# Kernel optimization log

Measured on AMD Instinct MI355X. Metric: run time of the kernel, lower is better.

Reference implementation:

```python
import jax, jax.numpy as jnp
import numpy as np

C = 16      # internal_channel
G = 8       # deform groups
KK = 9      # 3x3 kernel taps


def conv2d(x, w, b, pad):
    y = jax.lax.conv_general_dilated(
        x, w, window_strides=(1, 1), padding=[(pad, pad), (pad, pad)],
        dimension_numbers=('NCHW', 'OIHW', 'NCHW'))
    return y + b[None, :, None, None]


def feature_extraction(img, p):
    f1 = jax.nn.relu(conv2d(img, p['conv1_w'], p['conv1_b'], 1))   # [B,C,H,W]
    f2 = jax.nn.relu(conv2d(f1, p['conv2_w'], p['conv2_b'], 0))    # [B,C,H-2,W-2]
    f3 = jax.nn.relu(conv2d(f2, p['conv3_w'], p['conv3_b'], 0))    # [B,C,H-4,W-4]
    return [f1, f2, f3]


def deform_conv2d(x, offset, w, b, groups):
    # torchvision deform_conv2d semantics: stride 1, pad 1, dilation 1, 3x3,
    # zero out-of-bounds bilinear sampling, explicit offsets.
    B, Ci, H, W = x.shape
    Cg = Ci // groups
    off = offset.reshape(B, groups, KK, 2, H, W)
    oy, ox = off[:, :, :, 0], off[:, :, :, 1]          # [B,G,K,H,W]
    k = jnp.arange(KK)
    ky = (k // 3).reshape(1, 1, KK, 1, 1).astype(x.dtype)
    kx = (k % 3).reshape(1, 1, KK, 1, 1).astype(x.dtype)
    hh = jnp.arange(H, dtype=x.dtype).reshape(1, 1, 1, H, 1)
    ww = jnp.arange(W, dtype=x.dtype).reshape(1, 1, 1, 1, W)
    ys = hh - 1.0 + ky + oy                            # sample rows
    xs = ww - 1.0 + kx + ox                            # sample cols
    y0 = jnp.floor(ys); x0 = jnp.floor(xs)
    dy = ys - y0; dx = xs - x0
    y0i = y0.astype(jnp.int32); x0i = x0.astype(jnp.int32)
    xg = x.reshape(B, groups, Cg, H * W)

    def gather(iy, ix):
        valid = ((iy >= 0) & (iy < H) & (ix >= 0) & (ix < W)).astype(x.dtype)
        idx = jnp.clip(iy, 0, H - 1) * W + jnp.clip(ix, 0, W - 1)
        g = jnp.take_along_axis(xg, idx.reshape(B, groups, 1, KK * H * W), axis=3)
        return g.reshape(B, groups, Cg, KK, H, W) * valid[:, :, None]

    v = (gather(y0i, x0i) * ((1 - dy) * (1 - dx))[:, :, None]
         + gather(y0i, x0i + 1) * ((1 - dy) * dx)[:, :, None]
         + gather(y0i + 1, x0i) * (dy * (1 - dx))[:, :, None]
         + gather(y0i + 1, x0i + 1) * (dy * dx)[:, :, None])
    v = v.reshape(B, Ci, KK, H, W)
    out = jnp.einsum('ocK,bcKhw->bohw', w.reshape(w.shape[0], Ci, KK), v)
    return out + b[None, :, None, None]


def setup_inputs() -> dict:
    key = jax.random.key(0)
    ks = jax.random.split(key, 12)
    B, H, Wd = 4, 256, 256
    d = {
        'ref_image': jax.random.normal(ks[0], (B, 3, H, Wd), jnp.float32),
        'unreg_image': jax.random.normal(ks[1], (B, 3, H, Wd), jnp.float32),
        'conv1_w': jax.random.normal(ks[2], (C, 3, 3, 3), jnp.float32) * 0.05,
        'conv1_b': jnp.zeros((C,), jnp.float32),
        'conv2_w': jax.random.normal(ks[3], (C, C, 3, 3), jnp.float32) * 0.05,
        'conv2_b': jnp.zeros((C,), jnp.float32),
        'conv3_w': jax.random.normal(ks[4], (C, C, 3, 3), jnp.float32) * 0.05,
        'conv3_b': jnp.zeros((C,), jnp.float32),
        'off1_w': jax.random.normal(ks[5], (2 * G * KK, 2 * C, 3, 3), jnp.float32) * 0.01,
        'off1_b': jnp.zeros((2 * G * KK,), jnp.float32),
        'off2_w': jax.random.normal(ks[6], (2 * G * KK, 2 * C, 3, 3), jnp.float32) * 0.01,
        'off2_b': jnp.zeros((2 * G * KK,), jnp.float32),
        'off3_w': jax.random.normal(ks[7], (2 * G * KK, 2 * C, 3, 3), jnp.float32) * 0.01,
        'off3_b': jnp.zeros((2 * G * KK,), jnp.float32),
        'dcn_w': jax.random.normal(ks[8], (C, C, 3, 3), jnp.float32) * 0.05,
        'dcn_b': jnp.zeros((C,), jnp.float32),
    }
    return d


def reference(ref_image, unreg_image, conv1_w, conv1_b, conv2_w, conv2_b,
              conv3_w, conv3_b, off1_w, off1_b, off2_w, off2_b,
              off3_w, off3_b, dcn_w, dcn_b):
    p = dict(conv1_w=conv1_w, conv1_b=conv1_b, conv2_w=conv2_w, conv2_b=conv2_b,
             conv3_w=conv3_w, conv3_b=conv3_b)
    ref_f = feature_extraction(ref_image, p)
    unr_f = feature_extraction(unreg_image, p)
    off_ws = [(off1_w, off1_b), (off2_w, off2_b), (off3_w, off3_b)]
    aligned = []
    for i in range(3):
        cat = jnp.concatenate([ref_f[i], unr_f[i]], axis=1)          # [B,2C,Hi,Wi]
        offset = jax.nn.relu(conv2d(cat, off_ws[i][0], off_ws[i][1], 1))
        aligned.append(deform_conv2d(unr_f[i], offset, dcn_w, dcn_b, G))
    return tuple(aligned)
```

## Files before the change

### kernel.cpp

```cpp
#include <hip/hip_runtime.h>


typedef __attribute__((ext_vector_type(8))) short bf16x8;
typedef __attribute__((ext_vector_type(4))) float f32x4;
typedef __attribute__((ext_vector_type(2))) float f32x2;

__device__ inline unsigned short f2bf(float f) {
    union { float f; unsigned int u; } x; x.f = f;
    unsigned int u = x.u;
    u += 0x7fffu + ((u >> 16) & 1u);
    return (unsigned short)(u >> 16);
}
__device__ inline float bf2f(unsigned short u) {
    union { unsigned int i; float f; } x; x.i = ((unsigned int)u) << 16;
    return x.f;
}

__device__ inline void xcd_swz(int& bx, int& by, int& bz) {
    const int gx = gridDim.x, gy = gridDim.y, gz = gridDim.z;
    const int hw = blockIdx.x + gx * (blockIdx.y + gy * blockIdx.z);
    const int per = (gx * gy * gz) >> 3;
    const int lg = (hw & 7) * per + (hw >> 3);
    bz = lg / (gx * gy);
    const int rem = lg - bz * gx * gy;
    by = rem / gx;
    bx = rem - by * gx;
}

__global__ __launch_bounds__(256) void conv1_kernel(
    const float* __restrict__ ref, const float* __restrict__ unr,
    const float* __restrict__ w, const float* __restrict__ bias,
    float* __restrict__ outA, float* __restrict__ outB, float* __restrict__ pU)
{
    const int H = 256, W = 256;
    __shared__ float sIn[3][18][18];
    const int tx = threadIdx.x, ty = threadIdx.y;
    const int tid = ty * 16 + tx;
    const int bx = blockIdx.x, by = blockIdx.y, bz8 = blockIdx.z;
    const int isUnr = bz8 >> 2, bb = bz8 & 3;
    const float* in = isUnr ? unr : ref;
    float* outCL = isUnr ? outB : outA;
    const int x0 = bx * 16 - 1, y0 = by * 16 - 1;

    for (int idx = tid; idx < 3 * 324; idx += 256) {
        int c = idx / 324, rem = idx % 324, r = rem / 18, col = rem % 18;
        int gy = y0 + r, gx = x0 + col;
        float v = 0.f;
        if (gy >= 0 && gy < H && gx >= 0 && gx < W)
            v = in[((bb * 3 + c) * H + gy) * W + gx];
        sIn[c][r][col] = v;
    }
    __syncthreads();

    const int y = by * 16 + ty, x = bx * 16 + tx;
    float acc[16];
#pragma unroll
    for (int o = 0; o < 16; o++) acc[o] = bias[o];
#pragma unroll
    for (int ci = 0; ci < 3; ci++) {
        float xv[9];
#pragma unroll
        for (int r = 0; r < 3; r++)
#pragma unroll
            for (int c = 0; c < 3; c++)
                xv[r * 3 + c] = sIn[ci][ty + r][tx + c];
#pragma unroll
        for (int o = 0; o < 16; o++) {
            const float* wp = w + (o * 3 + ci) * 9;
#pragma unroll
            for (int u = 0; u < 9; u++) acc[o] += wp[u] * xv[u];
        }
    }
#pragma unroll
    for (int o = 0; o < 16; o++) acc[o] = fmaxf(acc[o], 0.f);

    const size_t HW = (size_t)H * W;
    float* op = outCL + ((size_t)bb * HW + (size_t)y * W + x) * 16;
#pragma unroll
    for (int i = 0; i < 4; ++i) {
        f32x4 v = {acc[4 * i], acc[4 * i + 1], acc[4 * i + 2], acc[4 * i + 3]};
        *(f32x4*)(op + 4 * i) = v;
    }
    if (isUnr) {
#pragma unroll
        for (int o = 0; o < 16; o++)
            pU[((size_t)(bb * 16 + o) * H + y) * W + x] = acc[o];
    }
}

__global__ __launch_bounds__(512, 4) void c16m_kernel(
    const float* __restrict__ inA, const float* __restrict__ inB,
    const unsigned short* __restrict__ Bc16, const float* __restrict__ bias,
    float* __restrict__ outA, float* __restrict__ outB, float* __restrict__ pU,
    int Hout, int Wout)
{
    const int Hin = Hout + 2, Win = Wout + 2;
    __shared__ __align__(16) unsigned short sC[324 * 16];
    __shared__ float sT[16][16][17];
    const int tid = threadIdx.x;
    const int bx = blockIdx.x, by = blockIdx.y, bz8 = blockIdx.z;
    const int isUnr = bz8 >> 2, bz = bz8 & 3;
    const float* inCL = isUnr ? inB : inA;
    float* outCL = isUnr ? outB : outA;
    const int x0 = bx * 16, y0 = by * 16;

    for (int idx = tid; idx < 324; idx += 512) {
        int r = idx / 18, c = idx % 18;
        int gy = min(y0 + r, Hin - 1), gx = min(x0 + c, Win - 1);
        const f32x4* p = (const f32x4*)(inCL + ((size_t)bz * Hin * Win + (size_t)gy * Win + gx) * 16);
        unsigned short tmp[16];
#pragma unroll
        for (int i = 0; i < 4; ++i) {
            f32x4 v = p[i];
            tmp[4 * i] = f2bf(v.x); tmp[4 * i + 1] = f2bf(v.y);
            tmp[4 * i + 2] = f2bf(v.z); tmp[4 * i + 3] = f2bf(v.w);
        }
        *(bf16x8*)&sC[idx * 16] = *(bf16x8*)&tmp[0];
        *(bf16x8*)&sC[idx * 16 + 8] = *(bf16x8*)&tmp[8];
    }
    __syncthreads();

    const int w = tid >> 6, l = tid & 63;
    const int q = l >> 4, j16 = l & 15;
    const float bv = bias[j16];
    f32x4 acc0 = {bv, bv, bv, bv}, acc1 = {bv, bv, bv, bv};

#pragma unroll
    for (int t = 0; t < 5; ++t) {
        const int u = (t == 4) ? 8 : 2 * t + (q >> 1);
        const int dr = u / 3, dc = u % 3;
        bf16x8 a0 = *(const bf16x8*)&sC[(((w) + dr) * 18 + (j16 + dc)) * 16 + (q & 1) * 8];
        bf16x8 a1 = *(const bf16x8*)&sC[(((w + 8) + dr) * 18 + (j16 + dc)) * 16 + (q & 1) * 8];
        bf16x8 b = *(const bf16x8*)&Bc16[(t * 64 + l) * 8];
        acc0 = __builtin_amdgcn_mfma_f32_16x16x32_bf16(a0, b, acc0, 0, 0, 0);
        acc1 = __builtin_amdgcn_mfma_f32_16x16x32_bf16(a1, b, acc1, 0, 0, 0);
    }
#pragma unroll
    for (int r = 0; r < 4; ++r) { acc0[r] = fmaxf(acc0[r], 0.f); acc1[r] = fmaxf(acc1[r], 0.f); }

    const int yA = y0 + w, yB = y0 + w + 8;
    const size_t HWo = (size_t)Hout * Wout;
#pragma unroll
    for (int r = 0; r < 4; ++r) {
        int x = x0 + 4 * q + r;
        if (yA < Hout && x < Wout)
            outCL[((size_t)bz * HWo + (size_t)yA * Wout + x) * 16 + j16] = acc0[r];
        if (yB < Hout && x < Wout)
            outCL[((size_t)bz * HWo + (size_t)yB * Wout + x) * 16 + j16] = acc1[r];
    }

    if (isUnr) {
#pragma unroll
        for (int r = 0; r < 4; ++r) {
            sT[w][j16][4 * q + r] = acc0[r];
            sT[w + 8][j16][4 * q + r] = acc1[r];
        }
        __syncthreads();
        const int ch = tid >> 5, yy = (tid >> 1) & 15, half = tid & 1;
        const int yo = y0 + yy;
        if (yo < Hout) {
            float* dst = pU + ((size_t)(bz * 16 + ch) * Hout + yo) * Wout + x0 + half * 8;
#pragma unroll
            for (int i = 0; i < 8; ++i) {
                int x = x0 + half * 8 + i;
                if (x < Wout) dst[i] = sT[yy][ch][half * 8 + i];
            }
        }
    }
}

__global__ __launch_bounds__(512) void prep_kernel(
    const float* __restrict__ o1w, const float* __restrict__ o2w, const float* __restrict__ o3w,
    const float* __restrict__ o1b, const float* __restrict__ o2b, const float* __restrict__ o3b,
    const float* __restrict__ dw, const float* __restrict__ c2w, const float* __restrict__ c3w,
    unsigned short* __restrict__ Bfrag, float* __restrict__ biasPrep, float* __restrict__ dwT,
    unsigned short* __restrict__ Bc16)
{
    const int lvl = blockIdx.y;
    const float* Wt = (lvl == 0) ? o1w : (lvl == 1) ? o2w : o3w;
    const float* Bb = (lvl == 0) ? o1b : (lvl == 1) ? o2b : o3b;
    int idx = blockIdx.x * 512 + threadIdx.x;
    int j = idx & 7;
    int l = (idx >> 3) & 63;
    int tu = idx >> 9;
    int t = tu / 9, u = tu % 9;
    int q = l >> 4, n16 = l & 15;
    int ci = 8 * q + j;
    int g = n16 >> 1, d = n16 & 1;
    int ch = g * 18 + t * 2 + d;
    Bfrag[lvl * 41472 + idx] = f2bf(Wt[(ch * 32 + ci) * 9 + u]);
    if (blockIdx.x == 0 && threadIdx.x < 144) {
        int n = threadIdx.x;
        int tt = n >> 4, nn = n & 15;
        biasPrep[lvl * 144 + n] = Bb[(nn >> 1) * 18 + tt * 2 + (nn & 1)];
    }
    if (lvl == 0 && blockIdx.x == 1) {
        for (int i = threadIdx.x; i < 2304; i += 512) {
            int c = i / 144, rem = i % 144, k = rem / 16, o = rem & 15;
            dwT[i] = dw[(o * 16 + c) * 9 + k];
        }
    }
    if (lvl == 2 && blockIdx.x >= 20 && blockIdx.x < 30) {
        int i2 = (blockIdx.x - 20) * 512 + threadIdx.x;
        int cw = i2 / 2560, rem = i2 % 2560;
        int jj = rem & 7, ll = (rem >> 3) & 63, tt = rem >> 9;
        int qq = ll >> 4, oo = ll & 15;
        int uu = (tt == 4) ? 8 : 2 * tt + (qq >> 1);
        int cc = (qq & 1) * 8 + jj;
        const float* wsel = cw ? c3w : c2w;
        float val = (tt == 4 && qq >= 2) ? 0.f : wsel[(oo * 16 + cc) * 9 + uu];
        Bc16[i2] = f2bf(val);
    }
}

#define CP 40
__global__ __launch_bounds__(512, 4) void offconv_kernel(
    const float* __restrict__ refCL, const float* __restrict__ unrCL,
    const unsigned short* __restrict__ Bfrag, const float* __restrict__ biasPrep,
    unsigned short* __restrict__ offbuf, int bbBase, int BN, int H, int W)
{
    __shared__ __align__(16) unsigned short sIn[18 * 18 * CP];
    const int tid = threadIdx.x;
    int bx, by, bz;
    xcd_swz(bx, by, bz);
    const int bb = bbBase + bz;
    const int x0 = bx * 16 - 1, y0 = by * 16 - 1;
    const size_t HW = (size_t)H * W;

    for (int idx = tid; idx < 648; idx += 512) {
        int px = idx >> 1, half = idx & 1;
        int r = px / 18, c = px % 18;
        int gy = y0 + r, gx = x0 + c;
        unsigned short tmp[16] = {0};
        if (gy >= 0 && gy < H && gx >= 0 && gx < W) {
            const float* src = half ? unrCL : refCL;
            const f32x4* p = (const f32x4*)(src + ((size_t)bb * HW + (size_t)gy * W + gx) * 16);
#pragma unroll
            for (int i = 0; i < 4; ++i) {
                f32x4 v = p[i];
                tmp[4 * i] = f2bf(v.x); tmp[4 * i + 1] = f2bf(v.y);
                tmp[4 * i + 2] = f2bf(v.z); tmp[4 * i + 3] = f2bf(v.w);
            }
        }
        *(bf16x8*)&sIn[px * CP + 16 * half] = *(bf16x8*)&tmp[0];
        *(bf16x8*)&sIn[px * CP + 16 * half + 8] = *(bf16x8*)&tmp[8];
    }
    __syncthreads();

    const int w = tid >> 6, l = tid & 63;
    const int q = l >> 4, j16 = l & 15;

    bf16x8 a0[9], a1[9];
#pragma unroll
    for (int u = 0; u < 9; ++u) {
        int dr = u / 3, dc = u % 3;
        a0[u] = *(const bf16x8*)&sIn[((w + dr) * 18 + (j16 + dc)) * CP + 8 * q];
        a1[u] = *(const bf16x8*)&sIn[((w + 8 + dr) * 18 + (j16 + dc)) * CP + 8 * q];
    }
    const int yA = by * 16 + w, yB = by * 16 + w + 8;

#pragma unroll 1
    for (int t = 0; t < 9; ++t) {
        float bv = biasPrep[t * 16 + j16];
        f32x4 acc0 = {bv, bv, bv, bv}, acc1 = {bv, bv, bv, bv};
#pragma unroll
        for (int u = 0; u < 9; ++u) {
            bf16x8 b = *(const bf16x8*)&Bfrag[((t * 9 + u) * 64 + l) * 8];
            acc0 = __builtin_amdgcn_mfma_f32_16x16x32_bf16(a0[u], b, acc0, 0, 0, 0);
            acc1 = __builtin_amdgcn_mfma_f32_16x16x32_bf16(a1[u], b, acc1, 0, 0, 0);
        }
        const size_t tb = ((size_t)t * BN + bz) * HW;
#pragma unroll
        for (int r = 0; r < 4; ++r) {
            int x = bx * 16 + 4 * q + r;
            if (yA < H && x < W)
                offbuf[(tb + (size_t)yA * W + x) * 16 + j16] = f2bf(fmaxf(acc0[r], 0.f));
            if (yB < H && x < W)
                offbuf[(tb + (size_t)yB * W + x) * 16 + j16] = f2bf(fmaxf(acc1[r], 0.f));
        }
    }
}

__global__ __launch_bounds__(256) void deform_kernel(
    const float* __restrict__ unrP, const unsigned short* __restrict__ offbuf,
    const float* __restrict__ dwT, const float* __restrict__ dcn_b,
    float* __restrict__ out, int bbBase, int BN, int H, int W)
{
    const int tx = threadIdx.x & 15, ty = threadIdx.x >> 4;
    int bxs, bys, bz;
    xcd_swz(bxs, bys, bz);
    const int bb = bbBase + bz;
    const int xr = bxs * 16 + tx, yr = bys * 16 + ty;
    const int x = min(xr, W - 1), y = min(yr, H - 1);
    const size_t HW = (size_t)H * W;
    const float* base = unrP + (size_t)bb * 16 * HW;
    const size_t pxi = (size_t)y * W + x;

    f32x4 pv[4];
#pragma unroll
    for (int i = 0; i < 4; ++i)
        pv[i] = (f32x4){dcn_b[4 * i], dcn_b[4 * i + 1], dcn_b[4 * i + 2], dcn_b[4 * i + 3]};

#pragma unroll 1
    for (int k = 0; k < 9; ++k) {
        const unsigned short* po = offbuf + (((size_t)k * BN + bz) * HW + pxi) * 16;
        bf16x8 s0 = *(const bf16x8*)(po);
        bf16x8 s1 = *(const bf16x8*)(po + 8);
        float ov[16];
#pragma unroll
        for (int i = 0; i < 8; ++i) ov[i] = bf2f((unsigned short)s0[i]);
#pragma unroll
        for (int i = 0; i < 8; ++i) ov[8 + i] = bf2f((unsigned short)s1[i]);

        const float fy = (float)(y - 1 + k / 3);
        const float fx = (float)(x - 1 + k % 3);
#pragma unroll
        for (int g = 0; g < 8; ++g) {
            float oy = ov[2 * g], ox = ov[2 * g + 1];
            float ys = fy + oy, xs = fx + ox;
            float y0f = floorf(ys), x0f = floorf(xs);
            float dy = ys - y0f, dx = xs - x0f;
            int iy0 = (int)y0f, ix0 = (int)x0f;
            int iy1 = iy0 + 1, ix1 = ix0 + 1;
            float vy0 = (iy0 >= 0 && iy0 < H) ? 1.f : 0.f;
            float vy1 = (iy1 >= 0 && iy1 < H) ? 1.f : 0.f;
            float vx0 = (ix0 >= 0 && ix0 < W) ? 1.f : 0.f;
            float vx1 = (ix1 >= 0 && ix1 < W) ? 1.f : 0.f;
            int cy0 = min(max(iy0, 0), H - 1), cy1 = min(max(iy1, 0), H - 1);
            int cx0 = min(max(ix0, 0), W - 1), cx1 = min(max(ix1, 0), W - 1);
            float w00 = (1.f - dy) * (1.f - dx) * vy0 * vx0;
            float w01 = (1.f - dy) * dx * vy0 * vx1;
            float w10 = dy * (1.f - dx) * vy1 * vx0;
            float w11 = dy * dx * vy1 * vx1;
            const float* p0 = base + (size_t)(2 * g) * HW;
            const float* p1 = base + (size_t)(2 * g + 1) * HW;
            const int i00 = cy0 * W + cx0, i01 = cy0 * W + cx1;
            const int i10 = cy1 * W + cx0, i11 = cy1 * W + cx1;
            f32x2 c00 = {p0[i00], p1[i00]}, c01 = {p0[i01], p1[i01]};
            f32x2 c10 = {p0[i10], p1[i10]}, c11 = {p0[i11], p1[i11]};
            f32x2 vv = w00 * c00 + w01 * c01 + w10 * c10 + w11 * c11;
            const f32x4* wv0 = (const f32x4*)(dwT + ((2 * g) * 9 + k) * 16);
            const f32x4* wv1 = (const f32x4*)(dwT + ((2 * g + 1) * 9 + k) * 16);
            const float v0 = vv.x, v1 = vv.y;
#pragma unroll
            for (int i = 0; i < 4; ++i) pv[i] += v0 * wv0[i];
#pragma unroll
            for (int i = 0; i < 4; ++i) pv[i] += v1 * wv1[i];
        }
    }

    if (xr < W && yr < H) {
#pragma unroll
        for (int i = 0; i < 4; ++i)
#pragma unroll
            for (int c = 0; c < 4; ++c)
                out[((size_t)(bb * 16 + 4 * i + c) * H + y) * W + x] = pv[i][c];
    }
}

extern "C" void kernel_launch(void* const* d_in, const int* in_sizes, int n_in,
                              void* d_out, int out_size, void* d_ws, size_t ws_size,
                              hipStream_t stream) {
    (void)in_sizes; (void)n_in; (void)out_size;
    const float* ref = (const float*)d_in[0];
    const float* unr = (const float*)d_in[1];
    const float* c1w = (const float*)d_in[2];  const float* c1b = (const float*)d_in[3];
    const float* c2w = (const float*)d_in[4];  const float* c2b = (const float*)d_in[5];
    const float* c3w = (const float*)d_in[6];  const float* c3b = (const float*)d_in[7];
    const float* o1w = (const float*)d_in[8];  const float* o1b = (const float*)d_in[9];
    const float* o2w = (const float*)d_in[10]; const float* o2b = (const float*)d_in[11];
    const float* o3w = (const float*)d_in[12]; const float* o3b = (const float*)d_in[13];
    const float* dw  = (const float*)d_in[14]; const float* db  = (const float*)d_in[15];

    float* out0 = (float*)d_out;
    float* out1 = out0 + (size_t)4 * 16 * 256 * 256;
    float* out2 = out1 + (size_t)4 * 16 * 254 * 254;

    float* fA = (float*)d_ws;
    float* fB = fA + (size_t)4 * 65536 * 16;
    float* fC = fB + (size_t)4 * 65536 * 16;
    float* fD = fC + (size_t)4 * 64516 * 16;
    float* pU = fD + (size_t)4 * 64516 * 16;
    unsigned short* BfragBase = (unsigned short*)(pU + (size_t)4 * 16 * 65536);
    unsigned short* Bc16 = BfragBase + 3 * 41472;
    float* biasPrep = (float*)(Bc16 + 2 * 2560);
    float* dwT = biasPrep + 3 * 144;
    unsigned short* offbuf = (unsigned short*)(dwT + 2304);

    const size_t used = (size_t)((char*)offbuf - (char*)d_ws);
    const size_t slice1 = (size_t)256 * 256 * 144;
    const int NB = (ws_size >= used + 4 * slice1 * 2) ? 4 : 1;

    dim3 blk(16, 16);
    prep_kernel<<<dim3(81, 3), 512, 0, stream>>>(o1w, o2w, o3w, o1b, o2b, o3b,
                                                 dw, c2w, c3w,
                                                 BfragBase, biasPrep, dwT, Bc16);
    conv1_kernel<<<dim3(16, 16, 8), blk, 0, stream>>>(ref, unr, c1w, c1b, fA, fB, pU);

    for (int lvl = 0; lvl < 3; ++lvl) {
        const float *rf, *uf; float* o; int H;
        const unsigned short* Bf = BfragBase + lvl * 41472;
        const float* bp = biasPrep + lvl * 144;
        if (lvl == 0) { rf = fA; uf = fB; o = out0; H = 256; }
        else if (lvl == 1) { rf = fC; uf = fD; o = out1; H = 254; }
        else { rf = fA; uf = fB; o = out2; H = 252; }

        if (NB == 4) {
            offconv_kernel<<<dim3(16, 16, 4), 512, 0, stream>>>(rf, uf, Bf, bp, offbuf, 0, 4, H, H);
            deform_kernel<<<dim3(16, 16, 4), 256, 0, stream>>>(pU, offbuf, dwT, db, o, 0, 4, H, H);
        } else {
            for (int b = 0; b < 4; ++b) {
                offconv_kernel<<<dim3(16, 16, 1), 512, 0, stream>>>(rf, uf, Bf, bp, offbuf, b, 1, H, H);
                deform_kernel<<<dim3(16, 16, 1), 256, 0, stream>>>(pU, offbuf, dwT, db, o, b, 1, H, H);
            }
        }

        if (lvl == 0) {
            c16m_kernel<<<dim3(16, 16, 8), 512, 0, stream>>>(fA, fB, Bc16, c2b, fC, fD, pU, 254, 254);
        } else if (lvl == 1) {
            c16m_kernel<<<dim3(16, 16, 8), 512, 0, stream>>>(fC, fD, Bc16 + 2560, c3b, fA, fB, pU, 252, 252);
        }
    }
}
```

Before: 383.0 us.

## Split deform groups across two thread halves with shared-memory reduction

Doubles the deform kernel's block to 512 threads and gives each half of the block four of the eight deform groups for the same pixel. Partial accumulators from the second half go through shared memory and are summed by the first half before the store. The aim is more parallelism and latency hiding for the gather-heavy bilinear sampling, and fewer registers per thread. The cost is a block-wide sync, about 20 KB of LDS per block, and each offset load split into two half-width loads.

```diff
diff --git a/kernel.cpp b/kernel.cpp
--- a/kernel.cpp
+++ b/kernel.cpp
@@ -281,12 +281,15 @@
     }
 }
 
-__global__ __launch_bounds__(256) void deform_kernel(
+__global__ __launch_bounds__(512, 4) void deform_kernel(
     const float* __restrict__ unrP, const unsigned short* __restrict__ offbuf,
     const float* __restrict__ dwT, const float* __restrict__ dcn_b,
     float* __restrict__ out, int bbBase, int BN, int H, int W)
 {
-    const int tx = threadIdx.x & 15, ty = threadIdx.x >> 4;
+    __shared__ float sRed[256 * 20];
+    const int tid = threadIdx.x;
+    const int px = tid & 255, half = tid >> 8;
+    const int tx = px & 15, ty = px >> 4;
     int bxs, bys, bz;
     xcd_swz(bxs, bys, bz);
     const int bb = bbBase + bz;
@@ -299,24 +302,23 @@
     f32x4 pv[4];
 #pragma unroll
     for (int i = 0; i < 4; ++i)
-        pv[i] = (f32x4){dcn_b[4 * i], dcn_b[4 * i + 1], dcn_b[4 * i + 2], dcn_b[4 * i + 3]};
+        pv[i] = half ? (f32x4){0.f, 0.f, 0.f, 0.f}
+                     : (f32x4){dcn_b[4 * i], dcn_b[4 * i + 1], dcn_b[4 * i + 2], dcn_b[4 * i + 3]};
 
 #pragma unroll 1
     for (int k = 0; k < 9; ++k) {
-        const unsigned short* po = offbuf + (((size_t)k * BN + bz) * HW + pxi) * 16;
-        bf16x8 s0 = *(const bf16x8*)(po);
-        bf16x8 s1 = *(const bf16x8*)(po + 8);
-        float ov[16];
-#pragma unroll
-        for (int i = 0; i < 8; ++i) ov[i] = bf2f((unsigned short)s0[i]);
-#pragma unroll
-        for (int i = 0; i < 8; ++i) ov[8 + i] = bf2f((unsigned short)s1[i]);
+        const unsigned short* po = offbuf + (((size_t)k * BN + bz) * HW + pxi) * 16 + half * 8;
+        bf16x8 s = *(const bf16x8*)po;
+        float ov[8];
+#pragma unroll
+        for (int i = 0; i < 8; ++i) ov[i] = bf2f((unsigned short)s[i]);
 
         const float fy = (float)(y - 1 + k / 3);
         const float fx = (float)(x - 1 + k % 3);
 #pragma unroll
-        for (int g = 0; g < 8; ++g) {
-            float oy = ov[2 * g], ox = ov[2 * g + 1];
+        for (int g4 = 0; g4 < 4; ++g4) {
+            const int g = half * 4 + g4;
+            float oy = ov[2 * g4], ox = ov[2 * g4 + 1];
             float ys = fy + oy, xs = fx + ox;
             float y0f = floorf(ys), x0f = floorf(xs);
             float dy = ys - y0f, dx = xs - x0f;
@@ -349,12 +351,19 @@
         }
     }
 
-    if (xr < W && yr < H) {
-#pragma unroll
-        for (int i = 0; i < 4; ++i)
+    if (half) {
+#pragma unroll
+        for (int i = 0; i < 4; ++i) *(f32x4*)&sRed[px * 20 + 4 * i] = pv[i];
+    }
+    __syncthreads();
+    if (!half && xr < W && yr < H) {
+#pragma unroll
+        for (int i = 0; i < 4; ++i) {
+            f32x4 o = pv[i] + *(const f32x4*)&sRed[px * 20 + 4 * i];
 #pragma unroll
             for (int c = 0; c < 4; ++c)
-                out[((size_t)(bb * 16 + 4 * i + c) * H + y) * W + x] = pv[i][c];
+                out[((size_t)(bb * 16 + 4 * i + c) * H + y) * W + x] = o[c];
+        }
     }
 }
 
@@ -407,11 +416,11 @@
 
         if (NB == 4) {
             offconv_kernel<<<dim3(16, 16, 4), 512, 0, stream>>>(rf, uf, Bf, bp, offbuf, 0, 4, H, H);
-            deform_kernel<<<dim3(16, 16, 4), 256, 0, stream>>>(pU, offbuf, dwT, db, o, 0, 4, H, H);
+            deform_kernel<<<dim3(16, 16, 4), 512, 0, stream>>>(pU, offbuf, dwT, db, o, 0, 4, H, H);
         } else {
             for (int b = 0; b < 4; ++b) {
                 offconv_kernel<<<dim3(16, 16, 1), 512, 0, stream>>>(rf, uf, Bf, bp, offbuf, b, 1, H, H);
-                deform_kernel<<<dim3(16, 16, 1), 256, 0, stream>>>(pU, offbuf, dwT, db, o, b, 1, H, H);
+                deform_kernel<<<dim3(16, 16, 1), 512, 0, stream>>>(pU, offbuf, dwT, db, o, b, 1, H, H);
             }
         }
 
```

Measured after the change: 535.5 us. 39.8% more time.
